# Performance work log

Measured on AMD Instinct MI355X. Metric: run time of the kernel, lower is better.

## Reference

```python
import jax, jax.numpy as jnp
import numpy as np
from itertools import combinations

# Static config (mirrors args / init_kwargs)
WAY, SHOT, SEQ_LEN, TSS = 5, 16, 10, 2
DIN, DOUT = 2048, 1152
N_QUERIES = 320
TUPLES = np.array(list(combinations(range(SEQ_LEN), TSS)), dtype=np.int32)  # [T, 2]
T = TUPLES.shape[0]  # 45
S = SHOT * T         # support tuples per class
OTHERS = np.array([[o for o in range(WAY) if o != c] for c in range(WAY)], dtype=np.int32)


def _cdist(a, b):
    # Euclidean distance matrix, [Na, Nb]
    d2 = (jnp.sum(a * a, axis=1)[:, None] + jnp.sum(b * b, axis=1)[None, :]
          - 2.0 * a @ b.T)
    return jnp.sqrt(jnp.maximum(d2, 1e-12))


def setup_inputs() -> dict:
    key = jax.random.key(0)
    k1, k2, k3 = jax.random.split(key, 3)
    support_set = jax.random.normal(k1, (WAY * SHOT, SEQ_LEN, DIN), jnp.float32)
    queries = jax.random.normal(k2, (N_QUERIES, SEQ_LEN, DIN), jnp.float32)
    support_labels = jnp.repeat(jnp.arange(WAY, dtype=jnp.int32), SHOT)
    W = jax.random.normal(k3, (DOUT, DIN * TSS), jnp.float32) / np.sqrt(DIN * TSS)
    b = jnp.zeros((DOUT,), jnp.float32)
    return {"support_set": support_set, "queries": queries,
            "support_labels": support_labels, "W": W, "b": b}


def reference(support_set, queries, support_labels, W, b):
    n_q = queries.shape[0]
    # Build frame-pair tuples: [N, T, TSS*DIN]  (dropout is identity in eval)
    sup_t = support_set[:, TUPLES, :].reshape(support_set.shape[0], T, TSS * DIN)
    q_t = queries[:, TUPLES, :].reshape(n_q, T, TSS * DIN)

    q_emb = jax.nn.relu(q_t.reshape(-1, TSS * DIN) @ W.T + b)          # [n_q*T, DOUT]
    order = jnp.argsort(support_labels).reshape(WAY, SHOT)             # class grouping
    class_sup = sup_t[order].reshape(WAY, S, TSS * DIN)
    sup_emb = jax.nn.relu(class_sup @ W.T + b)                          # [WAY, S, DOUT]

    dist_max_c, ave_all_c, pos_all_c = [], [], []
    for c in range(WAY):
        D = _cdist(q_emb, sup_emb[c])                                   # [n_q*T, S]
        # faithful to torch view(-1, T, shot).topk(k=1,dim=1).mean(dim=1)
        ave = D.reshape(-1, T, SHOT).max(axis=1).mean(axis=1)           # [n_q*T]
        dist_max_c.append(D.max(axis=1).reshape(n_q, T).mean(axis=1))   # [n_q]
        ave_all_c.append(ave)
        pos_all_c.append(jnp.argmax(D, axis=1))                         # [n_q*T]
    dist_max = jnp.stack(dist_max_c, axis=1)                            # [n_q, WAY]

    contrast_c = []
    for c in range(WAY):
        mse = sup_emb[c][pos_all_c[c]]                                  # [n_q*T, DOUT]
        so = sup_emb[OTHERS[c]]                                         # [WAY-1, S, DOUT]
        so_flat = so.reshape(-1, DOUT)
        CD = _cdist(mse, so_flat).reshape(-1, WAY - 1, S).transpose(1, 0, 2)  # [WAY-1, n_q*T, S]
        rec = (CD > ave_all_c[c][None, :, None]).sum(axis=1).astype(jnp.float32)  # [WAY-1, S]
        nz = jnp.maximum((rec > 0).sum(axis=1).astype(jnp.float32), 1.0)
        thr = rec.sum(axis=1) / nz
        mask = (rec < thr[:, None]).astype(jnp.float32).reshape(-1)     # [(WAY-1)*S]
        Dd = _cdist(q_emb, so_flat)                                     # [n_q*T, (WAY-1)*S]
        row = (Dd * mask).sum(axis=1) / jnp.maximum(mask.sum(), 1.0)    # masked mean == mean over gathered cols
        contrast_c.append(row.reshape(n_q, T).mean(axis=1) / (WAY - 1))
    dist_contrast = jnp.stack(contrast_c, axis=1)                       # [n_q, WAY]

    dist_sum = dist_contrast + dist_max
    logits_contrast = dist_max / dist_sum
    # (logits_max, logits_contrast) stacked: [2, n_q, WAY]
    return jnp.stack([dist_max, logits_contrast])
```

## Files before the change

kernel.cpp:

```cpp
#include <hip/hip_runtime.h>
#include <hip/hip_bf16.h>
#include <hip/hip_fp16.h>

#define WAY   5
#define SHOT  16
#define TT    45
#define SS    720
#define NQ    320
#define NQT   14400
#define NS    3600
#define MTOT  18000
#define DIN   2048
#define KDIM  4096
#define DOUT  1152
#define EROWS 18176
#define MAXIT 8192

#define QELT  (NQ * 10 * DIN)
#define SELT  (WAY * SHOT * 10 * DIN)
#define WELT  (DOUT * KDIM)

typedef __attribute__((ext_vector_type(8))) short bf16x8;
typedef __attribute__((ext_vector_type(8))) unsigned short u16x8;
typedef __attribute__((ext_vector_type(4))) float f32x4;

#define AS1 __attribute__((address_space(1)))
#define AS3 __attribute__((address_space(3)))

__constant__ unsigned char TUPI[TT] = {
  0,0,0,0,0,0,0,0,0, 1,1,1,1,1,1,1,1, 2,2,2,2,2,2,2,
  3,3,3,3,3,3, 4,4,4,4,4, 5,5,5,5, 6,6,6, 7,7, 8};
__constant__ unsigned char TUPJ[TT] = {
  1,2,3,4,5,6,7,8,9, 2,3,4,5,6,7,8,9, 3,4,5,6,7,8,9,
  4,5,6,7,8,9, 5,6,7,8,9, 6,7,8,9, 7,8,9, 8,9, 9};

__device__ inline unsigned short f2bf(float f) {
  union { float f; unsigned u; } v; v.f = f;
  unsigned r = v.u + 0x7FFFu + ((v.u >> 16) & 1u);
  return (unsigned short)(r >> 16);
}
__device__ inline float bf2f(unsigned short b) {
  union { unsigned u; float f; } v; v.u = ((unsigned)b) << 16;
  return v.f;
}
__device__ inline float h2f(unsigned short h) {
  union { __half h; unsigned short u; } v; v.u = h;
  return __half2float(v.h);
}
__device__ inline unsigned short f2h(float f) {
  union { __half h; unsigned short u; } v; v.h = __float2half(f);
  return v.u;
}

__device__ inline int xcd_swz(int o, int nwg) {
  int q = nwg >> 3, r = nwg & 7;
  int x = o & 7, i = o >> 3;
  return (x < r ? x * (q + 1) : r * (q + 1) + (x - r) * q) + i;
}

__global__ void sentinelK(float* __restrict__ out, float v) {
  int i = blockIdx.x * 256 + threadIdx.x;
  if (i < 2 * NQ * WAY) out[i] = v;
}

__global__ void packK(const float* __restrict__ qry, const float* __restrict__ sup,
                      const float* __restrict__ Wsrc,
                      unsigned short* __restrict__ qbf, unsigned short* __restrict__ sbf,
                      unsigned short* __restrict__ Wbf) {
  long long e = ((long long)blockIdx.x * 256 + threadIdx.x) * 8;
  const float* src; unsigned short* dst; long long o;
  if (e < QELT)                { src = qry;  dst = qbf; o = e; }
  else if (e < QELT + SELT)    { src = sup;  dst = sbf; o = e - QELT; }
  else if (e < QELT + SELT + WELT) { src = Wsrc; dst = Wbf; o = e - QELT - SELT; }
  else return;
  float4 a = *(const float4*)(src + o);
  float4 b = *(const float4*)(src + o + 4);
  u16x8 v;
  v[0] = f2bf(a.x); v[1] = f2bf(a.y); v[2] = f2bf(a.z); v[3] = f2bf(a.w);
  v[4] = f2bf(b.x); v[5] = f2bf(b.y); v[6] = f2bf(b.z); v[7] = f2bf(b.w);
  *(u16x8*)(dst + o) = v;
}

__global__ __launch_bounds__(256) void gemm1K(
    const unsigned short* __restrict__ qbf, const unsigned short* __restrict__ sbf,
    const unsigned short* __restrict__ Wbf, const float* __restrict__ bias,
    unsigned short* __restrict__ emb) {
  __shared__ unsigned short smem[16384];
  unsigned short* Alds = smem;
  unsigned short* Blds = smem + 8192;
  const int tid = threadIdx.x;
  const int lane = tid & 63;
  const int w = tid >> 6, wr = w >> 1, wc = w & 1;
  const int wg = xcd_swz(blockIdx.x, 141 * 9);
  const int bm = wg / 9, bn = wg % 9;

  const unsigned short* pAI[4];
  const unsigned short* pAJ[4];
  const unsigned short* pB[4];
  int ldso[4];
  const int cg8 = ((lane & 7) ^ (lane >> 3)) * 8;
  const unsigned short* Bbase = Wbf + (size_t)bn * 128 * KDIM;
#pragma unroll
  for (int i = 0; i < 4; ++i) {
    int row = w * 32 + i * 8 + (lane >> 3);
    int gr = bm * 128 + row;
    const unsigned short* base; int t;
    if (gr < NQT)       { t = gr % TT; base = qbf + (size_t)(gr / TT) * (10 * DIN); }
    else if (gr < MTOT) { int u = gr - NQT; int c = u / SS; int s = u % SS; t = s % TT;
                          base = sbf + (size_t)(c * SHOT + s / TT) * (10 * DIN); }
    else                { t = 0; base = qbf; }
    pAI[i] = base + (int)TUPI[t] * DIN + cg8;
    pAJ[i] = base + (int)TUPJ[t] * DIN + cg8;
    pB[i]  = Bbase + (size_t)row * KDIM + cg8;
    ldso[i] = __builtin_amdgcn_readfirstlane((w * 32 + i * 8) * 64);
  }
  const int l7 = lane & 7, c2b = lane >> 4;
  const int fo0 = (c2b ^ l7) << 3, fo1 = ((4 | c2b) ^ l7) << 3;
  int aoff[4], boff[4];
#pragma unroll
  for (int m = 0; m < 4; ++m) aoff[m] = (wr * 64 + m * 16 + (lane & 15)) * 64;
#pragma unroll
  for (int n = 0; n < 4; ++n) boff[n] = (wc * 64 + n * 16 + (lane & 15)) * 64;

  f32x4 acc[4][4] = {};

#pragma unroll
  for (int half = 0; half < 2; ++half) {
    const unsigned short* a0 = half ? pAJ[0] : pAI[0];
    const unsigned short* a1 = half ? pAJ[1] : pAI[1];
    const unsigned short* a2 = half ? pAJ[2] : pAI[2];
    const unsigned short* a3 = half ? pAJ[3] : pAI[3];
    const unsigned short* b0 = pB[0] + half * 2048;
    const unsigned short* b1 = pB[1] + half * 2048;
    const unsigned short* b2 = pB[2] + half * 2048;
    const unsigned short* b3 = pB[3] + half * 2048;
    for (int kt4 = 0; kt4 < 8; ++kt4) {
#pragma unroll
      for (int u = 0; u < 4; ++u) {
        __builtin_amdgcn_global_load_lds((const AS1 void*)(a0 + u * 64), (AS3 void*)(Alds + ldso[0]), 16, 0, 0);
        __builtin_amdgcn_global_load_lds((const AS1 void*)(a1 + u * 64), (AS3 void*)(Alds + ldso[1]), 16, 0, 0);
        __builtin_amdgcn_global_load_lds((const AS1 void*)(a2 + u * 64), (AS3 void*)(Alds + ldso[2]), 16, 0, 0);
        __builtin_amdgcn_global_load_lds((const AS1 void*)(a3 + u * 64), (AS3 void*)(Alds + ldso[3]), 16, 0, 0);
        __builtin_amdgcn_global_load_lds((const AS1 void*)(b0 + u * 64), (AS3 void*)(Blds + ldso[0]), 16, 0, 0);
        __builtin_amdgcn_global_load_lds((const AS1 void*)(b1 + u * 64), (AS3 void*)(Blds + ldso[1]), 16, 0, 0);
        __builtin_amdgcn_global_load_lds((const AS1 void*)(b2 + u * 64), (AS3 void*)(Blds + ldso[2]), 16, 0, 0);
        __builtin_amdgcn_global_load_lds((const AS1 void*)(b3 + u * 64), (AS3 void*)(Blds + ldso[3]), 16, 0, 0);
        __syncthreads();
#pragma unroll
        for (int kk = 0; kk < 2; ++kk) {
          const int fo = kk ? fo1 : fo0;
          bf16x8 af[4], bfr[4];
#pragma unroll
          for (int m = 0; m < 4; ++m) af[m] = *(const bf16x8*)(&Alds[aoff[m] + fo]);
#pragma unroll
          for (int n = 0; n < 4; ++n) bfr[n] = *(const bf16x8*)(&Blds[boff[n] + fo]);
#pragma unroll
          for (int m = 0; m < 4; ++m)
#pragma unroll
            for (int n = 0; n < 4; ++n)
              acc[m][n] = __builtin_amdgcn_mfma_f32_16x16x32_bf16(af[m], bfr[n], acc[m][n], 0, 0, 0);
        }
        __syncthreads();
      }
      a0 += 256; a1 += 256; a2 += 256; a3 += 256;
      b0 += 256; b1 += 256; b2 += 256; b3 += 256;
    }
  }

  const int lr0 = (lane >> 4) * 4;
  const int lc = lane & 15;
#pragma unroll
  for (int m = 0; m < 4; ++m)
#pragma unroll
    for (int n = 0; n < 4; ++n) {
      int lcol = wc * 64 + n * 16 + lc;
      float bv = bias[bn * 128 + lcol];
#pragma unroll
      for (int q = 0; q < 4; ++q) {
        int lrow = wr * 64 + m * 16 + lr0 + q;
        smem[lrow * 128 + (lcol ^ (((lrow >> 2) & 7) << 4))] =
            f2bf(fmaxf(acc[m][n][q] + bv, 0.0f));
      }
    }
  __syncthreads();
#pragma unroll
  for (int u8i = 0; u8i < 8; ++u8i) {
    int u = u8i * 256 + tid;
    int row = u >> 4, ch = u & 15;
    int gr = bm * 128 + row;
    if (gr < MTOT) {
      u16x8 v = *(const u16x8*)(&smem[row * 128 + ((ch * 8) ^ (((row >> 2) & 7) << 4))]);
      *(u16x8*)(&emb[(size_t)gr * DOUT + bn * 128 + ch * 8]) = v;
    }
  }
}

__global__ __launch_bounds__(256) void gemm2K(
    const unsigned short* __restrict__ emb, const float* __restrict__ norms,
    __half* __restrict__ Dh) {
  __shared__ unsigned short smem[32768];
  const int tid = threadIdx.x;
  const int lane = tid & 63;
  const int w = tid >> 6, wr = w >> 1, wc = w & 1;
  const int wg = xcd_swz(blockIdx.x, 141 * 29);
  const int grp = wg / (8 * 29);
  const int rem = wg % (8 * 29);
  const int gsz = min(8, 141 - grp * 8);
  const int bm = grp * 8 + rem % gsz;
  const int bn = rem / gsz;

  const unsigned short* pA[4];
  const unsigned short* pB[4];
  int ldso[4];
  const int cg8 = ((lane & 7) ^ (lane >> 3)) * 8;
  const unsigned short* Abase = emb + (size_t)bm * 128 * DOUT;
  const unsigned short* Bbase = emb + (size_t)(NQT + bn * 128) * DOUT;
#pragma unroll
  for (int i = 0; i < 4; ++i) {
    int row = w * 32 + i * 8 + (lane >> 3);
    pA[i] = Abase + (size_t)row * DOUT + cg8;
    pB[i] = Bbase + (size_t)row * DOUT + cg8;
    ldso[i] = __builtin_amdgcn_readfirstlane((w * 32 + i * 8) * 64);
  }
  const int l7 = lane & 7, c2b = lane >> 4;
  const int fo0 = (c2b ^ l7) << 3, fo1 = ((4 | c2b) ^ l7) << 3;
  int aoff[4], boff[4];
#pragma unroll
  for (int m = 0; m < 4; ++m) aoff[m] = (wr * 64 + m * 16 + (lane & 15)) * 64;
#pragma unroll
  for (int n = 0; n < 4; ++n) boff[n] = (wc * 64 + n * 16 + (lane & 15)) * 64;

  f32x4 acc[4][4] = {};

  auto stage = [&](int kt, int buf) {
    unsigned short* ab = smem + (buf << 14);
    unsigned short* bb = ab + 8192;
    __builtin_amdgcn_global_load_lds((const AS1 void*)(pA[0] + kt * 64), (AS3 void*)(ab + ldso[0]), 16, 0, 0);
    __builtin_amdgcn_global_load_lds((const AS1 void*)(pA[1] + kt * 64), (AS3 void*)(ab + ldso[1]), 16, 0, 0);
    __builtin_amdgcn_global_load_lds((const AS1 void*)(pA[2] + kt * 64), (AS3 void*)(ab + ldso[2]), 16, 0, 0);
    __builtin_amdgcn_global_load_lds((const AS1 void*)(pA[3] + kt * 64), (AS3 void*)(ab + ldso[3]), 16, 0, 0);
    __builtin_amdgcn_global_load_lds((const AS1 void*)(pB[0] + kt * 64), (AS3 void*)(bb + ldso[0]), 16, 0, 0);
    __builtin_amdgcn_global_load_lds((const AS1 void*)(pB[1] + kt * 64), (AS3 void*)(bb + ldso[1]), 16, 0, 0);
    __builtin_amdgcn_global_load_lds((const AS1 void*)(pB[2] + kt * 64), (AS3 void*)(bb + ldso[2]), 16, 0, 0);
    __builtin_amdgcn_global_load_lds((const AS1 void*)(pB[3] + kt * 64), (AS3 void*)(bb + ldso[3]), 16, 0, 0);
  };
  auto compute = [&](int buf) {
    const unsigned short* ca = smem + (buf << 14);
    const unsigned short* cb = ca + 8192;
#pragma unroll
    for (int kk = 0; kk < 2; ++kk) {
      const int fo = kk ? fo1 : fo0;
      bf16x8 af[4], bfr[4];
#pragma unroll
      for (int m = 0; m < 4; ++m) af[m] = *(const bf16x8*)(&ca[aoff[m] + fo]);
#pragma unroll
      for (int n = 0; n < 4; ++n) bfr[n] = *(const bf16x8*)(&cb[boff[n] + fo]);
#pragma unroll
      for (int m = 0; m < 4; ++m)
#pragma unroll
        for (int n = 0; n < 4; ++n)
          acc[m][n] = __builtin_amdgcn_mfma_f32_16x16x32_bf16(af[m], bfr[n], acc[m][n], 0, 0, 0);
    }
  };

  stage(0, 0);
  asm volatile("s_waitcnt vmcnt(0)" ::: "memory");
  __builtin_amdgcn_sched_barrier(0);
  __builtin_amdgcn_s_barrier();
#pragma unroll
  for (int kt = 1; kt < DOUT / 64; ++kt) {
    stage(kt, kt & 1);
    asm volatile("s_waitcnt vmcnt(8)" ::: "memory");
    __builtin_amdgcn_sched_barrier(0);
    __builtin_amdgcn_s_barrier();
    compute((kt - 1) & 1);
    __builtin_amdgcn_s_barrier();
  }
  asm volatile("s_waitcnt vmcnt(0)" ::: "memory");
  __builtin_amdgcn_sched_barrier(0);
  __builtin_amdgcn_s_barrier();
  compute(1);
  __syncthreads();

  const int lr0 = (lane >> 4) * 4;
  const int lc = lane & 15;
#pragma unroll
  for (int m = 0; m < 4; ++m)
#pragma unroll
    for (int n = 0; n < 4; ++n) {
      int lcol = wc * 64 + n * 16 + lc;
      float nb_ = norms[NQT + bn * 128 + lcol];
#pragma unroll
      for (int q = 0; q < 4; ++q) {
        int lrow = wr * 64 + m * 16 + lr0 + q;
        float d2 = norms[bm * 128 + lrow] + nb_ - 2.0f * acc[m][n][q];
        smem[lrow * 128 + (lcol ^ (((lrow >> 2) & 7) << 4))] =
            f2h(sqrtf(fmaxf(d2, 1e-12f)));
      }
    }
  __syncthreads();
  unsigned short* Dhu = (unsigned short*)Dh;
#pragma unroll
  for (int u8i = 0; u8i < 8; ++u8i) {
    int u = u8i * 256 + tid;
    int row = u >> 4, ch = u & 15;
    int gr = bm * 128 + row;
    int gc0 = bn * 128 + ch * 8;
    if (gr < MTOT && gc0 < NS) {
      u16x8 v = *(const u16x8*)(&smem[row * 128 + ((ch * 8) ^ (((row >> 2) & 7) << 4))]);
      *(u16x8*)(&Dhu[(size_t)gr * NS + gc0]) = v;
    }
  }
}

__global__ void normK(const unsigned short* __restrict__ emb, float* __restrict__ norms) {
  int row = blockIdx.x * 4 + (threadIdx.x >> 6);
  int lane = threadIdx.x & 63;
  const unsigned short* e = emb + (size_t)row * DOUT;
  float acc = 0.f;
  u16x8 x0 = *(const u16x8*)(e + lane * 8);
  u16x8 x1 = *(const u16x8*)(e + 512 + lane * 8);
#pragma unroll
  for (int k = 0; k < 8; ++k) {
    float a = bf2f(x0[k]); acc += a * a;
    float b = bf2f(x1[k]); acc += b * b;
  }
  unsigned t = *(const unsigned*)(e + 1024 + lane * 2);
  float c0 = bf2f((unsigned short)(t & 0xFFFFu)); acc += c0 * c0;
  float c1 = bf2f((unsigned short)(t >> 16));     acc += c1 * c1;
  for (int sh = 1; sh < 64; sh <<= 1) acc += __shfl_xor(acc, sh);
  if (lane == 0) norms[row] = acc;
}

__global__ void passA(const __half* __restrict__ Dh, float* __restrict__ rowmax,
                      float* __restrict__ ave, int* __restrict__ pos) {
  int wid = blockIdx.x * 4 + (threadIdx.x >> 6);
  int lane = threadIdx.x & 63;
  int c = wid / NQT, r = wid % NQT;
  const unsigned short* row = (const unsigned short*)(Dh + (size_t)r * NS + c * SS);
  u16x8 v0 = *(const u16x8*)(row + lane * 8);
  bool act1 = lane < 26;
  u16x8 v1 = v0;
  if (act1) v1 = *(const u16x8*)(row + 512 + lane * 8);
  float m8[8];
  unsigned pm = 0;
#pragma unroll
  for (int k = 0; k < 8; ++k) {
    unsigned h0 = v0[k];
    int col0 = lane * 8 + k;
    unsigned p0 = (h0 << 16) | (unsigned)(65535 - col0);
    pm = pm > p0 ? pm : p0;
    m8[k] = h2f((unsigned short)h0);
  }
  if (act1) {
#pragma unroll
    for (int k = 0; k < 8; ++k) {
      unsigned h1 = v1[k];
      int col1 = 512 + lane * 8 + k;
      unsigned p1 = (h1 << 16) | (unsigned)(65535 - col1);
      pm = pm > p1 ? pm : p1;
      m8[k] = fmaxf(m8[k], h2f((unsigned short)h1));
    }
  }
  for (int sh = 1; sh < 64; sh <<= 1) {
    unsigned o = (unsigned)__shfl_xor((int)pm, sh);
    pm = pm > o ? pm : o;
  }
  for (int sh = 2; sh < 64; sh <<= 1) {
#pragma unroll
    for (int k = 0; k < 8; ++k)
      m8[k] = fmaxf(m8[k], __shfl_xor(m8[k], sh));
  }
  float sj = ((m8[0] + m8[1]) + (m8[2] + m8[3])) + ((m8[4] + m8[5]) + (m8[6] + m8[7]));
  sj += __shfl_xor(sj, 1);
  if (lane == 0) {
    rowmax[c * NQT + r] = h2f((unsigned short)(pm >> 16));
    ave[c * NQT + r] = sj * (1.0f / 16.0f);
    pos[c * NQT + r] = 65535 - (int)(pm & 0xFFFFu);
  }
}

__global__ void bucketCntK(const int* __restrict__ pos, unsigned* __restrict__ bcnt) {
  __shared__ unsigned h[NS];
  int tid = threadIdx.x;
  for (int i = tid; i < NS; i += 256) h[i] = 0;
  __syncthreads();
  for (int idx = blockIdx.x * 256 + tid; idx < WAY * NQT; idx += gridDim.x * 256) {
    int c = idx / NQT;
    atomicAdd(&h[c * SS + pos[idx]], 1u);
  }
  __syncthreads();
  for (int i = tid; i < NS; i += 256) {
    unsigned v = h[i];
    if (v) atomicAdd(&bcnt[i], v);
  }
}

__global__ void pfxItemsK(const unsigned* __restrict__ bcnt, unsigned* __restrict__ bstart,
                          unsigned* __restrict__ nitems, unsigned* __restrict__ items) {
  __shared__ unsigned s[1024];
  int c = blockIdx.x, tid = threadIdx.x;
  for (int i = tid; i < 1024; i += 256) s[i] = (i < SS) ? bcnt[c * SS + i] : 0u;
  __syncthreads();
  for (int off = 1; off < 1024; off <<= 1) {
    unsigned v[4];
#pragma unroll
    for (int k = 0; k < 4; ++k) { int i = tid + k * 256; v[k] = (i >= off) ? s[i - off] : 0u; }
    __syncthreads();
#pragma unroll
    for (int k = 0; k < 4; ++k) { int i = tid + k * 256; s[i] += v[k]; }
    __syncthreads();
  }
  for (int i = tid; i < SS; i += 256) {
    unsigned excl = (i ? s[i - 1] : 0u);
    bstart[c * SS + i] = excl;
    unsigned nb = s[i] - excl;
    if (nb) {
      unsigned ni = (nb + 63) >> 6;
      unsigned base = atomicAdd(nitems, ni);
      for (unsigned k = 0; k < ni; ++k) items[base + k] = ((unsigned)(c * SS + i) << 8) | k;
    }
  }
}

__global__ void bucketSctK(const int* __restrict__ pos, const float* __restrict__ ave,
                           const unsigned* __restrict__ bstart, unsigned* __restrict__ bfill,
                           float* __restrict__ bav) {
  int idx = blockIdx.x * 256 + threadIdx.x;
  if (idx >= WAY * NQT) return;
  int c = idx / NQT;
  int p = pos[idx];
  unsigned j = atomicAdd(&bfill[c * SS + p], 1u);
  bav[c * NQT + bstart[c * SS + p] + j] = ave[idx];
}

__global__ __launch_bounds__(256) void recK4(const __half* __restrict__ Dh,
                                             const unsigned* __restrict__ bstart,
                                             const unsigned* __restrict__ bcnt,
                                             const float* __restrict__ bav,
                                             const unsigned* __restrict__ items,
                                             const unsigned* __restrict__ nitems,
                                             unsigned* __restrict__ rec) {
  int lane = threadIdx.x & 63, wv = threadIdx.x >> 6;
  int nit = (int)nitems[0];
  int nw = gridDim.x * 4;
  for (int i = blockIdx.x * 4 + wv; i < nit; i += nw) {
    unsigned it = items[i];
    int cp = (int)(it >> 8), k = (int)(it & 255u);
    int c = cp / SS, p = cp % SS;
    int c0 = c * SS;
    int b0 = (int)bstart[cp], nb = (int)bcnt[cp];
    int j0 = k << 6;
    float av = (j0 + lane < nb) ? bav[c * NQT + b0 + j0 + lane] : 3.0e38f;
    const __half* row = Dh + (size_t)(NQT + c0 + p) * NS;
    for (int itr = 0; itr < 45; ++itr) {
      int os = itr * 64 + lane;
      int col = os + ((os >= c0) ? SS : 0);
      float v = __half2float(row[col]);
      unsigned cnt = 0;
#pragma unroll 16
      for (int j = 0; j < 64; ++j)
        cnt += (v > __shfl(av, j)) ? 1u : 0u;
      if (cnt) atomicAdd(&rec[c * 2880 + os], cnt);
    }
  }
}

__global__ void maskK(const unsigned* __restrict__ rec, float* __restrict__ maskfull,
                      float* __restrict__ nmask) {
  int c = blockIdx.x;
  int tid = threadIdx.x, lane = tid & 63, wv = tid >> 6;
  __shared__ float thr[WAY - 1];
  __shared__ float red[8];
  for (int o = 0; o < WAY - 1; ++o) {
    float s = 0.f, nz = 0.f;
    for (int i = tid; i < SS; i += 256) {
      unsigned v = rec[c * (WAY - 1) * SS + o * SS + i];
      s += (float)v;
      if (v > 0u) nz += 1.f;
    }
    for (int sh = 1; sh < 64; sh <<= 1) { s += __shfl_xor(s, sh); nz += __shfl_xor(nz, sh); }
    if (lane == 0) { red[wv] = s; red[4 + wv] = nz; }
    __syncthreads();
    if (tid == 0) thr[o] = (red[0] + red[1] + red[2] + red[3]) /
                           fmaxf(red[4] + red[5] + red[6] + red[7], 1.0f);
    __syncthreads();
  }
  float cntm = 0.f;
  for (int col = tid; col < NS; col += 256) {
    float mv = 0.f;
    int cb = col / SS;
    if (cb != c) {
      int os = col - ((col >= (c + 1) * SS) ? SS : 0);
      mv = (((float)rec[c * (WAY - 1) * SS + os]) < thr[os / SS]) ? 1.f : 0.f;
    }
    maskfull[c * NS + col] = mv;
    cntm += mv;
  }
  for (int sh = 1; sh < 64; sh <<= 1) cntm += __shfl_xor(cntm, sh);
  if (lane == 0) red[wv] = cntm;
  __syncthreads();
  if (tid == 0) nmask[c] = red[0] + red[1] + red[2] + red[3];
}

__global__ void mask5K(const float* __restrict__ maskfull, unsigned char* __restrict__ mask5) {
  int col = blockIdx.x * 256 + threadIdx.x;
  if (col >= NS) return;
  unsigned m = 0;
#pragma unroll
  for (int c = 0; c < WAY; ++c)
    m |= (maskfull[c * NS + col] > 0.5f) ? (1u << c) : 0u;
  mask5[col] = (unsigned char)m;
}

__global__ void passB(const __half* __restrict__ Dh, const unsigned char* __restrict__ mask5,
                      const float* __restrict__ nmask, float* __restrict__ row5) {
  int r = blockIdx.x * 4 + (threadIdx.x >> 6);
  int lane = threadIdx.x & 63;
  const unsigned short* drow = (const unsigned short*)(Dh + (size_t)r * NS);
  float a[WAY] = {0.f, 0.f, 0.f, 0.f, 0.f};
#pragma unroll
  for (int it = 0; it < 8; ++it) {
    int col = it * 512 + lane * 8;
    if (col < NS) {
      u16x8 v = *(const u16x8*)(drow + col);
      unsigned long long mb = *(const unsigned long long*)(mask5 + col);
#pragma unroll
      for (int k = 0; k < 8; ++k) {
        float f = h2f(v[k]);
        unsigned m = (unsigned)(mb >> (8 * k)) & 31u;
#pragma unroll
        for (int c = 0; c < WAY; ++c) a[c] += ((m >> c) & 1u) ? f : 0.f;
      }
    }
  }
#pragma unroll
  for (int c = 0; c < WAY; ++c)
    for (int sh = 1; sh < 64; sh <<= 1) a[c] += __shfl_xor(a[c], sh);
  if (lane == 0)
#pragma unroll
    for (int c = 0; c < WAY; ++c)
      row5[(size_t)r * WAY + c] = a[c] / fmaxf(nmask[c], 1.0f);
}

__global__ void finalK(const float* __restrict__ rowmax, const float* __restrict__ row5,
                       float* __restrict__ out) {
  int idx = blockIdx.x * 256 + threadIdx.x;
  if (idx >= NQ * WAY) return;
  int q = idx / WAY, c = idx % WAY;
  float sm = 0.f, sc = 0.f;
  for (int t = 0; t < TT; ++t) {
    int r = q * TT + t;
    sm += rowmax[c * NQT + r];
    sc += row5[(size_t)r * WAY + c];
  }
  float dm = sm / 45.0f;
  float ctr = sc / 45.0f * 0.25f;
  out[idx] = dm;
  out[NQ * WAY + idx] = dm / (ctr + dm);
}

extern "C" void kernel_launch(void* const* d_in, const int* in_sizes, int n_in,
                              void* d_out, int out_size, void* d_ws, size_t ws_size,
                              hipStream_t stream) {
  const float* sup  = (const float*)d_in[0];
  const float* qry  = (const float*)d_in[1];
  const float* Wsrc = (const float*)d_in[3];
  const float* bias = (const float*)d_in[4];
  float* out = (float*)d_out;

  char* base = (char*)d_ws;
  size_t off = 0;
  __half* Dh = (__half*)(base + off);                  off += (size_t)MTOT * NS * 2;
  unsigned short* qbf = (unsigned short*)Dh;
  unsigned short* sbf = qbf + QELT;
  unsigned short* Wbf = sbf + SELT;
  unsigned short* emb = (unsigned short*)(base + off); off += (size_t)EROWS * DOUT * 2;
  float* norms  = (float*)(base + off);   off += (size_t)EROWS * 4;
  float* rowmax = (float*)(base + off);   off += (size_t)WAY * NQT * 4;
  float* ave    = (float*)(base + off);   off += (size_t)WAY * NQT * 4;
  int*   pos    = (int*)(base + off);     off += (size_t)WAY * NQT * 4;
  char* zbase = base + off;
  unsigned* rec    = (unsigned*)(base + off); off += (size_t)WAY * (WAY - 1) * SS * 4;
  unsigned* bcnt   = (unsigned*)(base + off); off += (size_t)WAY * SS * 4;
  unsigned* bfill  = (unsigned*)(base + off); off += (size_t)WAY * SS * 4;
  unsigned* nitems = (unsigned*)(base + off); off += 64;
  size_t zbytes = (size_t)((base + off) - zbase);
  unsigned* bstart = (unsigned*)(base + off); off += (size_t)WAY * SS * 4;
  float* maskfull = (float*)(base + off); off += (size_t)WAY * NS * 4;
  unsigned char* mask5 = (unsigned char*)(base + off); off += 4096;
  float* nmask  = (float*)(base + off);   off += 64;
  float* row5   = (float*)(base + off);   off += (size_t)NQT * WAY * 4;
  float* bav    = (float*)(base + off);   off += (size_t)WAY * NQT * 4;
  unsigned* items = (unsigned*)(base + off); off += MAXIT * 4;

  if (ws_size < off) {
    sentinelK<<<13, 256, 0, stream>>>(out, -(1000.0f + (float)(ws_size >> 20)));
    return;
  }

  (void)hipMemsetAsync(zbase, 0, zbytes, stream);
  packK<<<6304, 256, 0, stream>>>(qry, sup, Wsrc, qbf, sbf, Wbf);
  gemm1K<<<141 * 9, 256, 0, stream>>>(qbf, sbf, Wbf, bias, emb);
  normK<<<4500, 256, 0, stream>>>(emb, norms);
  gemm2K<<<141 * 29, 256, 0, stream>>>(emb, norms, Dh);
  passA<<<18000, 256, 0, stream>>>(Dh, rowmax, ave, pos);
  bucketCntK<<<282, 256, 0, stream>>>(pos, bcnt);
  pfxItemsK<<<WAY, 256, 0, stream>>>(bcnt, bstart, nitems, items);
  bucketSctK<<<282, 256, 0, stream>>>(pos, ave, bstart, bfill, bav);
  recK4<<<1184, 256, 0, stream>>>(Dh, bstart, bcnt, bav, items, nitems, rec);
  maskK<<<WAY, 256, 0, stream>>>(rec, maskfull, nmask);
  mask5K<<<15, 256, 0, stream>>>(maskfull, mask5);
  passB<<<3600, 256, 0, stream>>>(Dh, mask5, nmask, row5);
  finalK<<<7, 256, 0, stream>>>(rowmax, row5, out);
}
```

Measured before the change: 577.4 us.

## Double-buffer LDS in embedding GEMM to overlap global loads with MFMA

The embedding GEMM's main loop now uses two LDS buffers. The next K-tile is issued with global_load_lds while MFMAs run on the current tile, and a partial vmcnt wait plus barriers keep the two in step. The earlier loop did load, sync, compute, sync with nothing overlapped, so global latency was exposed on every step. In exchange LDS use doubles to 64KB per block, which may reduce occupancy.

```diff
diff --git a/kernel.cpp b/kernel.cpp
--- a/kernel.cpp
+++ b/kernel.cpp
@@ -85,9 +85,7 @@
     const unsigned short* __restrict__ qbf, const unsigned short* __restrict__ sbf,
     const unsigned short* __restrict__ Wbf, const float* __restrict__ bias,
     unsigned short* __restrict__ emb) {
-  __shared__ unsigned short smem[16384];
-  unsigned short* Alds = smem;
-  unsigned short* Blds = smem + 8192;
+  __shared__ unsigned short smem[32768];
   const int tid = threadIdx.x;
   const int lane = tid & 63;
   const int w = tid >> 6, wr = w >> 1, wc = w & 1;
@@ -96,10 +94,13 @@
 
   const unsigned short* pAI[4];
   const unsigned short* pAJ[4];
-  const unsigned short* pB[4];
   int ldso[4];
   const int cg8 = ((lane & 7) ^ (lane >> 3)) * 8;
   const unsigned short* Bbase = Wbf + (size_t)bn * 128 * KDIM;
+  const unsigned short* b0;
+  const unsigned short* b1;
+  const unsigned short* b2;
+  const unsigned short* b3;
 #pragma unroll
   for (int i = 0; i < 4; ++i) {
     int row = w * 32 + i * 8 + (lane >> 3);
@@ -111,8 +112,14 @@
     else                { t = 0; base = qbf; }
     pAI[i] = base + (int)TUPI[t] * DIN + cg8;
     pAJ[i] = base + (int)TUPJ[t] * DIN + cg8;
-    pB[i]  = Bbase + (size_t)row * KDIM + cg8;
     ldso[i] = __builtin_amdgcn_readfirstlane((w * 32 + i * 8) * 64);
+  }
+  {
+    int row0 = w * 32 + (lane >> 3);
+    b0 = Bbase + (size_t)(row0)      * KDIM + cg8;
+    b1 = Bbase + (size_t)(row0 + 8)  * KDIM + cg8;
+    b2 = Bbase + (size_t)(row0 + 16) * KDIM + cg8;
+    b3 = Bbase + (size_t)(row0 + 24) * KDIM + cg8;
   }
   const int l7 = lane & 7, c2b = lane >> 4;
   const int fo0 = (c2b ^ l7) << 3, fo1 = ((4 | c2b) ^ l7) << 3;
@@ -124,48 +131,62 @@
 
   f32x4 acc[4][4] = {};
 
-#pragma unroll
-  for (int half = 0; half < 2; ++half) {
-    const unsigned short* a0 = half ? pAJ[0] : pAI[0];
-    const unsigned short* a1 = half ? pAJ[1] : pAI[1];
-    const unsigned short* a2 = half ? pAJ[2] : pAI[2];
-    const unsigned short* a3 = half ? pAJ[3] : pAI[3];
-    const unsigned short* b0 = pB[0] + half * 2048;
-    const unsigned short* b1 = pB[1] + half * 2048;
-    const unsigned short* b2 = pB[2] + half * 2048;
-    const unsigned short* b3 = pB[3] + half * 2048;
-    for (int kt4 = 0; kt4 < 8; ++kt4) {
-#pragma unroll
-      for (int u = 0; u < 4; ++u) {
-        __builtin_amdgcn_global_load_lds((const AS1 void*)(a0 + u * 64), (AS3 void*)(Alds + ldso[0]), 16, 0, 0);
-        __builtin_amdgcn_global_load_lds((const AS1 void*)(a1 + u * 64), (AS3 void*)(Alds + ldso[1]), 16, 0, 0);
-        __builtin_amdgcn_global_load_lds((const AS1 void*)(a2 + u * 64), (AS3 void*)(Alds + ldso[2]), 16, 0, 0);
-        __builtin_amdgcn_global_load_lds((const AS1 void*)(a3 + u * 64), (AS3 void*)(Alds + ldso[3]), 16, 0, 0);
-        __builtin_amdgcn_global_load_lds((const AS1 void*)(b0 + u * 64), (AS3 void*)(Blds + ldso[0]), 16, 0, 0);
-        __builtin_amdgcn_global_load_lds((const AS1 void*)(b1 + u * 64), (AS3 void*)(Blds + ldso[1]), 16, 0, 0);
-        __builtin_amdgcn_global_load_lds((const AS1 void*)(b2 + u * 64), (AS3 void*)(Blds + ldso[2]), 16, 0, 0);
-        __builtin_amdgcn_global_load_lds((const AS1 void*)(b3 + u * 64), (AS3 void*)(Blds + ldso[3]), 16, 0, 0);
-        __syncthreads();
-#pragma unroll
-        for (int kk = 0; kk < 2; ++kk) {
-          const int fo = kk ? fo1 : fo0;
-          bf16x8 af[4], bfr[4];
-#pragma unroll
-          for (int m = 0; m < 4; ++m) af[m] = *(const bf16x8*)(&Alds[aoff[m] + fo]);
-#pragma unroll
-          for (int n = 0; n < 4; ++n) bfr[n] = *(const bf16x8*)(&Blds[boff[n] + fo]);
-#pragma unroll
-          for (int m = 0; m < 4; ++m)
-#pragma unroll
-            for (int n = 0; n < 4; ++n)
-              acc[m][n] = __builtin_amdgcn_mfma_f32_16x16x32_bf16(af[m], bfr[n], acc[m][n], 0, 0, 0);
-        }
-        __syncthreads();
-      }
-      a0 += 256; a1 += 256; a2 += 256; a3 += 256;
-      b0 += 256; b1 += 256; b2 += 256; b3 += 256;
-    }
-  }
+  const unsigned short* a0 = pAI[0];
+  const unsigned short* a1 = pAI[1];
+  const unsigned short* a2 = pAI[2];
+  const unsigned short* a3 = pAI[3];
+
+  auto stage = [&](int buf) {
+    unsigned short* ab = smem + (buf << 14);
+    unsigned short* bb = ab + 8192;
+    __builtin_amdgcn_global_load_lds((const AS1 void*)a0, (AS3 void*)(ab + ldso[0]), 16, 0, 0); a0 += 64;
+    __builtin_amdgcn_global_load_lds((const AS1 void*)a1, (AS3 void*)(ab + ldso[1]), 16, 0, 0); a1 += 64;
+    __builtin_amdgcn_global_load_lds((const AS1 void*)a2, (AS3 void*)(ab + ldso[2]), 16, 0, 0); a2 += 64;
+    __builtin_amdgcn_global_load_lds((const AS1 void*)a3, (AS3 void*)(ab + ldso[3]), 16, 0, 0); a3 += 64;
+    __builtin_amdgcn_global_load_lds((const AS1 void*)b0, (AS3 void*)(bb + ldso[0]), 16, 0, 0); b0 += 64;
+    __builtin_amdgcn_global_load_lds((const AS1 void*)b1, (AS3 void*)(bb + ldso[1]), 16, 0, 0); b1 += 64;
+    __builtin_amdgcn_global_load_lds((const AS1 void*)b2, (AS3 void*)(bb + ldso[2]), 16, 0, 0); b2 += 64;
+    __builtin_amdgcn_global_load_lds((const AS1 void*)b3, (AS3 void*)(bb + ldso[3]), 16, 0, 0); b3 += 64;
+  };
+  auto compute = [&](int buf) {
+    const unsigned short* ca = smem + (buf << 14);
+    const unsigned short* cb = ca + 8192;
+#pragma unroll
+    for (int kk = 0; kk < 2; ++kk) {
+      const int fo = kk ? fo1 : fo0;
+      bf16x8 af[4], bfr[4];
+#pragma unroll
+      for (int m = 0; m < 4; ++m) af[m] = *(const bf16x8*)(&ca[aoff[m] + fo]);
+#pragma unroll
+      for (int n = 0; n < 4; ++n) bfr[n] = *(const bf16x8*)(&cb[boff[n] + fo]);
+#pragma unroll
+      for (int m = 0; m < 4; ++m)
+#pragma unroll
+        for (int n = 0; n < 4; ++n)
+          acc[m][n] = __builtin_amdgcn_mfma_f32_16x16x32_bf16(af[m], bfr[n], acc[m][n], 0, 0, 0);
+    }
+  };
+
+  stage(0);
+  asm volatile("s_waitcnt vmcnt(0)" ::: "memory");
+  __builtin_amdgcn_sched_barrier(0);
+  __builtin_amdgcn_s_barrier();
+  int cur = 0;
+  for (int kt = 1; kt < KDIM / 64; ++kt) {
+    if (kt == 32) { a0 = pAJ[0]; a1 = pAJ[1]; a2 = pAJ[2]; a3 = pAJ[3]; }
+    stage(cur ^ 1);
+    asm volatile("s_waitcnt vmcnt(8)" ::: "memory");
+    __builtin_amdgcn_sched_barrier(0);
+    __builtin_amdgcn_s_barrier();
+    compute(cur);
+    __builtin_amdgcn_s_barrier();
+    cur ^= 1;
+  }
+  asm volatile("s_waitcnt vmcnt(0)" ::: "memory");
+  __builtin_amdgcn_sched_barrier(0);
+  __builtin_amdgcn_s_barrier();
+  compute(cur);
+  __syncthreads();
 
   const int lr0 = (lane >> 4) * 4;
   const int lc = lane & 15;
```

Result: faster. 545.9 us (median of 2 runs) (-5.5%).
